# Performance work log

Measured on AMD Instinct MI355X. Metric: run time of the kernel, lower is better.

Reference implementation:

```python
import jax, jax.numpy as jnp
import numpy as np

DIM = 1024
NUM_HEADS = 16
HEAD_DIM = DIM // NUM_HEADS
SCALE = HEAD_DIM ** (-0.5)


def setup_inputs() -> dict:
    key = jax.random.key(0)
    ks = jax.random.split(key, 5)
    B, N, C = 2, 2048, DIM
    q = jax.random.normal(ks[0], (B, N, C), dtype=jnp.float32)
    k = jax.random.normal(ks[1], (B, N, C), dtype=jnp.float32)
    v = jax.random.normal(ks[2], (B, N, C), dtype=jnp.float32)
    # fused qkv Linear weight, torch layout [3*C, C]; no bias (qkv_bias=False)
    qkv_w = jax.random.normal(ks[3], (3 * C, C), dtype=jnp.float32) * (C ** -0.5)
    proj_w = jax.random.normal(ks[4], (C, C), dtype=jnp.float32) * (C ** -0.5)
    proj_b = jnp.zeros((C,), dtype=jnp.float32)
    return {"q": q, "k": k, "v": v, "qkv_w": qkv_w, "proj_w": proj_w,
            "proj_b": proj_b, "use_mask": 1}


def reference(q, k, v, qkv_w, proj_w, proj_b, use_mask):
    B, N, C = q.shape
    N_k = k.shape[1]
    H, hd = NUM_HEADS, HEAD_DIM
    # The original applies the full fused qkv Linear to each of q,k,v and keeps
    # only slice 0/1/2 respectively; computing just the used slice is identical math.
    wq, wk, wv = qkv_w[:C], qkv_w[C:2 * C], qkv_w[2 * C:]
    qh = (q @ wq.T).reshape(B, N, H, hd).transpose(0, 2, 1, 3)      # [B,H,N,hd]
    kh = (k @ wk.T).reshape(B, N_k, H, hd).transpose(0, 2, 1, 3)    # [B,H,Nk,hd]
    vh = (v @ wv.T).reshape(B, N_k, H, hd).transpose(0, 2, 1, 3)    # [B,H,Nk,hd]
    attn = jnp.einsum('bhnd,bhmd->bhnm', qh, kh) * SCALE            # [B,H,N,Nk]
    if use_mask:  # static Python flag -> causal tril mask as in the source
        msk = jnp.tril(jnp.ones((N, N_k), dtype=bool))
        attn = jnp.where(msk[None, None], attn, jnp.float32(-1e9))
    attn = jax.nn.softmax(attn, axis=-1)
    x = jnp.einsum('bhnm,bhmd->bhnd', attn, vh)                     # [B,H,N,hd]
    x = x.transpose(0, 2, 1, 3).reshape(B, N, C)
    x = x @ proj_w.T + proj_b
    return x, attn
```

## Files before the change

### kernel.cpp

```cpp
#include <hip/hip_runtime.h>


typedef unsigned short u16;
typedef unsigned int u32;
typedef __attribute__((ext_vector_type(8))) short s16x8;
typedef __attribute__((ext_vector_type(4))) float f32x4;
typedef __attribute__((ext_vector_type(4))) u16 u16x4;

#define AS1 __attribute__((address_space(1)))
#define AS3 __attribute__((address_space(3)))

static __device__ __forceinline__ u16 f2bf(float f) {
  u32 u = __builtin_bit_cast(u32, f);
  u = (u + 0x7fffu + ((u >> 16) & 1u)) >> 16;
  return (u16)u;
}

static __device__ __forceinline__ void gll16(const u16* g, u16* l) {
  __builtin_amdgcn_global_load_lds((const AS1 u32*)g, (AS3 u32*)l, 16, 0, 0);
}

static __device__ __forceinline__ f32x4 mfma_bf16(s16x8 a, s16x8 b, f32x4 c) {
  return __builtin_amdgcn_mfma_f32_16x16x32_bf16(a, b, c, 0, 0, 0);
}

__global__ __launch_bounds__(256) void cast_kernel(const float* __restrict__ in,
                                                   u16* __restrict__ out, int n4) {
  int i = blockIdx.x * 256 + threadIdx.x;
  if (i < n4) {
    f32x4 v = ((const f32x4*)in)[i];
    u16x4 o = { f2bf(v.x), f2bf(v.y), f2bf(v.z), f2bf(v.w) };
    ((u16x4*)out)[i] = o;
  }
}

static __device__ __forceinline__ void gemm_core_1024(
    const u16* __restrict__ A, const u16* __restrict__ Bm,
    int m0, int n0, int t, u16* a_s, u16* b_s, f32x4 acc[4][4]) {
  const int lane = t & 63;
  const int w = t >> 6;
  const int wm = (w & 1) * 64, wn = (w >> 1) * 64;
  const int lrow = lane & 15, lq = lane >> 4;
  const int r0 = t >> 2;
  const int c0 = (t & 3) * 8;

  for (int kt = 0; kt < 1024; kt += 32) {
    __syncthreads();
    gll16(A  + (size_t)(m0 + r0)      * 1024 + kt + c0, &a_s[(size_t)t * 8]);
    gll16(A  + (size_t)(m0 + r0 + 64) * 1024 + kt + c0, &a_s[(size_t)(t + 256) * 8]);
    gll16(Bm + (size_t)(n0 + r0)      * 1024 + kt + c0, &b_s[(size_t)t * 8]);
    gll16(Bm + (size_t)(n0 + r0 + 64) * 1024 + kt + c0, &b_s[(size_t)(t + 256) * 8]);
    __syncthreads();
    s16x8 af[4], bfr[4];
#pragma unroll
    for (int x = 0; x < 4; x++) af[x]  = *(const s16x8*)&a_s[(wm + x*16 + lrow)*32 + lq*8];
#pragma unroll
    for (int x = 0; x < 4; x++) bfr[x] = *(const s16x8*)&b_s[(wn + x*16 + lrow)*32 + lq*8];
#pragma unroll
    for (int tm = 0; tm < 4; tm++)
#pragma unroll
      for (int tn = 0; tn < 4; tn++)
        acc[tm][tn] = mfma_bf16(af[tm], bfr[tn], acc[tm][tn]);
  }
}

__global__ __launch_bounds__(256) void gemm_qkv_kernel(
    const u16* __restrict__ qb, const u16* __restrict__ kb, const u16* __restrict__ vb,
    const u16* __restrict__ wb, u16* __restrict__ Qh, u16* __restrict__ Kh,
    u16* __restrict__ Vt) {
  __shared__ u16 a_s[128*32], b_s[128*32];
  const int mode = blockIdx.z;
  const u16* A = (mode == 0) ? qb : (mode == 1) ? kb : vb;
  const u16* Bm = wb + (size_t)mode * (1024 * 1024);
  const int m0 = blockIdx.y * 128, n0 = blockIdx.x * 128;
  const int t = threadIdx.x;
  f32x4 acc[4][4];
  const f32x4 Z = {0.f, 0.f, 0.f, 0.f};
#pragma unroll
  for (int i = 0; i < 4; i++)
#pragma unroll
    for (int j = 0; j < 4; j++) acc[i][j] = Z;

  gemm_core_1024(A, Bm, m0, n0, t, a_s, b_s, acc);

  const int lane = t & 63, w = t >> 6;
  const int wm = (w & 1) * 64, wn = (w >> 1) * 64;
  const int lrow = lane & 15, lq = lane >> 4;
#pragma unroll
  for (int tm = 0; tm < 4; tm++) {
#pragma unroll
    for (int tn = 0; tn < 4; tn++) {
      const int ng = n0 + wn + tn * 16 + lrow;
      const int h = ng >> 6, d = ng & 63;
#pragma unroll
      for (int i = 0; i < 4; i++) {
        const int mg = m0 + wm + tm * 16 + lq * 4 + i;
        const int b = mg >> 11, s = mg & 2047;
        const float v = acc[tm][tn][i];
        if (mode == 0)
          Qh[((size_t)(b * 16 + h) * 2048 + s) * 64 + d] = f2bf(v * 0.125f);
        else if (mode == 1)
          Kh[((size_t)(b * 16 + h) * 2048 + s) * 64 + d] = f2bf(v);
        else
          Vt[((size_t)(b * 16 + h) * 64 + d) * 2048 + s] = f2bf(v);
      }
    }
  }
}

__global__ __launch_bounds__(256) void gemm_proj_kernel(
    const u16* __restrict__ xatt, const u16* __restrict__ pwb,
    const float* __restrict__ bias, float* __restrict__ out) {
  __shared__ u16 a_s[128*32], b_s[128*32];
  const int m0 = blockIdx.y * 128, n0 = blockIdx.x * 128;
  const int t = threadIdx.x;
  f32x4 acc[4][4];
  const f32x4 Z = {0.f, 0.f, 0.f, 0.f};
#pragma unroll
  for (int i = 0; i < 4; i++)
#pragma unroll
    for (int j = 0; j < 4; j++) acc[i][j] = Z;

  gemm_core_1024(xatt, pwb, m0, n0, t, a_s, b_s, acc);

  const int lane = t & 63, w = t >> 6;
  const int wm = (w & 1) * 64, wn = (w >> 1) * 64;
  const int lrow = lane & 15, lq = lane >> 4;
#pragma unroll
  for (int tn = 0; tn < 4; tn++) {
    const int ng = n0 + wn + tn * 16 + lrow;
    const float bv = bias[ng];
#pragma unroll
    for (int tm = 0; tm < 4; tm++) {
#pragma unroll
      for (int i = 0; i < 4; i++) {
        const int mg = m0 + wm + tm * 16 + lq * 4 + i;
        out[(size_t)mg * 1024 + ng] = acc[tm][tn][i] + bv;
      }
    }
  }
}

__global__ __launch_bounds__(256) void attn_kernel(
    const u16* __restrict__ Qh, const u16* __restrict__ Kh, const u16* __restrict__ Vt,
    float* __restrict__ attn, u16* __restrict__ xatt, const int* __restrict__ use_mask_p) {
  __shared__ u16 q_s[64*64], k_s[64*64], v_s[64*64];
  __shared__ u16 p_s[4][16*64];

  const int bh = blockIdx.y;
  const int q0 = blockIdx.x * 64;
  const int t = threadIdx.x;
  const int lane = t & 63, w = t >> 6;
  const int lrow = lane & 15, lq = lane >> 4;
  const int use_mask = *use_mask_p;
  const int T = use_mask ? (q0 >> 6) : 31;

  const int rs = t >> 3;
  const int cs = (t & 7) * 8;

  const u16* qg = Qh + ((size_t)bh * 2048 + q0) * 64;
  gll16(qg + (size_t)rs * 64 + cs,        &q_s[(size_t)t * 8]);
  gll16(qg + (size_t)(rs + 32) * 64 + cs, &q_s[(size_t)(t + 256) * 8]);
  __syncthreads();

  s16x8 qf[2];
#pragma unroll
  for (int kq = 0; kq < 2; kq++)
    qf[kq] = *(const s16x8*)&q_s[(w * 16 + lrow) * 64 + kq * 32 + lq * 8];

  const u16* kg = Kh + (size_t)bh * (2048 * 64);
  const u16* vg = Vt + (size_t)bh * (64 * 2048);

  float l_acc[4] = {0.f, 0.f, 0.f, 0.f};
  for (int tt = 0; tt <= T; tt++) {
    __syncthreads();
    gll16(kg + (size_t)(tt * 64 + rs) * 64 + cs,      &k_s[(size_t)t * 8]);
    gll16(kg + (size_t)(tt * 64 + rs + 32) * 64 + cs, &k_s[(size_t)(t + 256) * 8]);
    __syncthreads();
    f32x4 sacc[4];
    const f32x4 Z = {0.f, 0.f, 0.f, 0.f};
#pragma unroll
    for (int tn = 0; tn < 4; tn++) {
      sacc[tn] = Z;
#pragma unroll
      for (int kq = 0; kq < 2; kq++) {
        s16x8 kf = *(const s16x8*)&k_s[(tn * 16 + lrow) * 64 + kq * 32 + lq * 8];
        sacc[tn] = mfma_bf16(qf[kq], kf, sacc[tn]);
      }
    }
    const bool diag = use_mask && (tt == T);
    float part[4] = {0.f, 0.f, 0.f, 0.f};
#pragma unroll
    for (int tn = 0; tn < 4; tn++)
#pragma unroll
      for (int i = 0; i < 4; i++) {
        const bool ok = !diag || (tn * 16 + lrow <= w * 16 + lq * 4 + i);
        part[i] += ok ? __expf(sacc[tn][i]) : 0.f;
      }
#pragma unroll
    for (int i = 0; i < 4; i++) {
      float p = part[i];
      p += __shfl_xor(p, 1, 16);
      p += __shfl_xor(p, 2, 16);
      p += __shfl_xor(p, 4, 16);
      p += __shfl_xor(p, 8, 16);
      l_acc[i] += p;
    }
  }
  float inv_l[4];
#pragma unroll
  for (int i = 0; i < 4; i++) inv_l[i] = 1.0f / l_acc[i];

  f32x4 oacc[4];
  const f32x4 Z = {0.f, 0.f, 0.f, 0.f};
#pragma unroll
  for (int i = 0; i < 4; i++) oacc[i] = Z;

  for (int tt = 0; tt <= T; tt++) {
    __syncthreads();
    gll16(kg + (size_t)(tt * 64 + rs) * 64 + cs,      &k_s[(size_t)t * 8]);
    gll16(kg + (size_t)(tt * 64 + rs + 32) * 64 + cs, &k_s[(size_t)(t + 256) * 8]);
    gll16(vg + (size_t)rs * 2048 + tt * 64 + cs,        &v_s[(size_t)t * 8]);
    gll16(vg + (size_t)(rs + 32) * 2048 + tt * 64 + cs, &v_s[(size_t)(t + 256) * 8]);
    __syncthreads();
    f32x4 sacc[4];
#pragma unroll
    for (int tn = 0; tn < 4; tn++) {
      sacc[tn] = Z;
#pragma unroll
      for (int kq = 0; kq < 2; kq++) {
        s16x8 kf = *(const s16x8*)&k_s[(tn * 16 + lrow) * 64 + kq * 32 + lq * 8];
        sacc[tn] = mfma_bf16(qf[kq], kf, sacc[tn]);
      }
    }
    const bool diag = use_mask && (tt == T);
    float* abase = attn + ((size_t)(bh * 2048 + q0 + w * 16)) * 2048 + tt * 64;
#pragma unroll
    for (int tn = 0; tn < 4; tn++)
#pragma unroll
      for (int i = 0; i < 4; i++) {
        const bool ok = !diag || (tn * 16 + lrow <= w * 16 + lq * 4 + i);
        const float p = ok ? __expf(sacc[tn][i]) * inv_l[i] : 0.f;
        const int rl = lq * 4 + i;
        abase[(size_t)rl * 2048 + tn * 16 + lrow] = p;
        p_s[w][rl * 64 + tn * 16 + lrow] = f2bf(p);
      }
    s16x8 pf[2];
#pragma unroll
    for (int kq = 0; kq < 2; kq++)
      pf[kq] = *(const s16x8*)&p_s[w][lrow * 64 + kq * 32 + lq * 8];
#pragma unroll
    for (int td = 0; td < 4; td++)
#pragma unroll
      for (int kq = 0; kq < 2; kq++) {
        s16x8 vf = *(const s16x8*)&v_s[(td * 16 + lrow) * 64 + kq * 32 + lq * 8];
        oacc[td] = mfma_bf16(pf[kq], vf, oacc[td]);
      }
  }

  const int b = bh >> 4, h = bh & 15;
#pragma unroll
  for (int td = 0; td < 4; td++)
#pragma unroll
    for (int i = 0; i < 4; i++) {
      const int row = q0 + w * 16 + lq * 4 + i;
      xatt[((size_t)(b * 2048 + row)) * 1024 + h * 64 + td * 16 + lrow] = f2bf(oacc[td][i]);
    }

  if (use_mask) {
    const int zc0 = q0 + 64;
    if (zc0 < 2048) {
      const int nzv = (2048 - zc0) >> 2;
      f32x4* zb = (f32x4*)(attn + ((size_t)bh * 2048 + q0) * 2048 + zc0);
      const int row = t >> 2;
      const f32x4 Z4 = {0.f, 0.f, 0.f, 0.f};
      for (int c = (t & 3); c < nzv; c += 4)
        zb[(size_t)row * 512 + c] = Z4;
    }
  }
}

extern "C" void kernel_launch(void* const* d_in, const int* in_sizes, int n_in,
                              void* d_out, int out_size, void* d_ws, size_t ws_size,
                              hipStream_t stream) {
  const float* q      = (const float*)d_in[0];
  const float* k      = (const float*)d_in[1];
  const float* v      = (const float*)d_in[2];
  const float* qkv_w  = (const float*)d_in[3];
  const float* proj_w = (const float*)d_in[4];
  const float* proj_b = (const float*)d_in[5];
  const int*   use_mask = (const int*)d_in[6];

  const size_t MB = 1024 * 1024;
  char* ws = (char*)d_ws;
  u16* qb  = (u16*)(ws + 0 * MB);
  u16* kb  = (u16*)(ws + 8 * MB);
  u16* vb  = (u16*)(ws + 16 * MB);
  u16* wb  = (u16*)(ws + 24 * MB);
  u16* pwb = (u16*)(ws + 30 * MB);
  u16* Qh  = (u16*)(ws + 32 * MB);
  u16* Kh  = (u16*)(ws + 40 * MB);
  u16* Vt  = (u16*)(ws + 48 * MB);
  u16* xat = qb;

  float* out_x    = (float*)d_out;
  float* out_attn = out_x + (size_t)2 * 2048 * 1024;

  cast_kernel<<<4096, 256, 0, stream>>>(q, qb, 1048576);
  cast_kernel<<<4096, 256, 0, stream>>>(k, kb, 1048576);
  cast_kernel<<<4096, 256, 0, stream>>>(v, vb, 1048576);
  cast_kernel<<<3072, 256, 0, stream>>>(qkv_w, wb, 786432);
  cast_kernel<<<1024, 256, 0, stream>>>(proj_w, pwb, 262144);

  gemm_qkv_kernel<<<dim3(8, 32, 3), 256, 0, stream>>>(qb, kb, vb, wb, Qh, Kh, Vt);
  attn_kernel<<<dim3(32, 32), 256, 0, stream>>>(Qh, Kh, Vt, out_attn, xat, use_mask);
  gemm_proj_kernel<<<dim3(8, 32), 256, 0, stream>>>(xat, pwb, proj_b, out_x);
}
```

Before: 772.8 us.

## Pair causal query tiles per block with double-buffered swizzled K/V loads

Each attention block now handles two query tiles, p and 31-p, so causal work is balanced across blocks and every K/V tile loaded into LDS serves both. K and V loads are double-buffered so the next tile is fetched during compute, and LDS is XOR-swizzled, with the P scratch padded to cut bank conflicts. MFMA sections are wrapped in s_setprio. The grid is halved, which reduces block count and parallelism, and register pressure rises from holding two sets of accumulators.

```diff
diff --git a/kernel.cpp b/kernel.cpp
--- a/kernel.cpp
+++ b/kernel.cpp
@@ -141,141 +141,239 @@
   }
 }
 
+
+static __device__ __forceinline__ void qk_tile(const s16x8 qf[2], const s16x8 kf[4][2],
+                                               f32x4 sacc[4]) {
+  const f32x4 Z = {0.f, 0.f, 0.f, 0.f};
+#pragma unroll
+  for (int tn = 0; tn < 4; tn++) {
+    sacc[tn] = Z;
+#pragma unroll
+    for (int kq = 0; kq < 2; kq++)
+      sacc[tn] = mfma_bf16(qf[kq], kf[tn][kq], sacc[tn]);
+  }
+}
+
+static __device__ __forceinline__ void expsum_tile(const f32x4 sacc[4], bool diag,
+                                                   int lrow, int rbase, float l_acc[4]) {
+  float part[4] = {0.f, 0.f, 0.f, 0.f};
+#pragma unroll
+  for (int tn = 0; tn < 4; tn++)
+#pragma unroll
+    for (int i = 0; i < 4; i++) {
+      const bool ok = !diag || (tn * 16 + lrow <= rbase + i);
+      part[i] += ok ? __expf(sacc[tn][i]) : 0.f;
+    }
+#pragma unroll
+  for (int i = 0; i < 4; i++) {
+    float s = part[i];
+    s += __shfl_xor(s, 1, 16);
+    s += __shfl_xor(s, 2, 16);
+    s += __shfl_xor(s, 4, 16);
+    s += __shfl_xor(s, 8, 16);
+    l_acc[i] += s;
+  }
+}
+
+static __device__ __forceinline__ void p_tile(const f32x4 sacc[4], bool diag, int lrow,
+                                              int lq, int w, const float inv_l[4],
+                                              float* __restrict__ abase, u16* p_w,
+                                              s16x8 pf[2]) {
+#pragma unroll
+  for (int tn = 0; tn < 4; tn++)
+#pragma unroll
+    for (int i = 0; i < 4; i++) {
+      const int rl = lq * 4 + i;
+      const bool ok = !diag || (tn * 16 + lrow <= w * 16 + rl);
+      const float pv = ok ? __expf(sacc[tn][i]) * inv_l[i] : 0.f;
+      abase[(size_t)rl * 2048 + tn * 16 + lrow] = pv;
+      p_w[rl * 72 + tn * 16 + lrow] = f2bf(pv);
+    }
+#pragma unroll
+  for (int kq = 0; kq < 2; kq++)
+    pf[kq] = *(const s16x8*)&p_w[lrow * 72 + kq * 32 + lq * 8];
+}
+
 __global__ __launch_bounds__(256) void attn_kernel(
     const u16* __restrict__ Qh, const u16* __restrict__ Kh, const u16* __restrict__ Vt,
     float* __restrict__ attn, u16* __restrict__ xatt, const int* __restrict__ use_mask_p) {
-  __shared__ u16 q_s[64*64], k_s[64*64], v_s[64*64];
-  __shared__ u16 p_s[4][16*64];
+  __shared__ u16 smem[8192 + 8192 + 8 * 16 * 72];
+  u16* k_s = smem;
+  u16* vq  = smem + 8192;
+  u16* p_s = smem + 16384;
 
   const int bh = blockIdx.y;
-  const int q0 = blockIdx.x * 64;
+  const int p  = blockIdx.x;
   const int t = threadIdx.x;
   const int lane = t & 63, w = t >> 6;
   const int lrow = lane & 15, lq = lane >> 4;
   const int use_mask = *use_mask_p;
-  const int T = use_mask ? (q0 >> 6) : 31;
-
-  const int rs = t >> 3;
-  const int cs = (t & 7) * 8;
-
-  const u16* qg = Qh + ((size_t)bh * 2048 + q0) * 64;
-  gll16(qg + (size_t)rs * 64 + cs,        &q_s[(size_t)t * 8]);
-  gll16(qg + (size_t)(rs + 32) * 64 + cs, &q_s[(size_t)(t + 256) * 8]);
-  __syncthreads();
-
-  s16x8 qf[2];
-#pragma unroll
-  for (int kq = 0; kq < 2; kq++)
-    qf[kq] = *(const s16x8*)&q_s[(w * 16 + lrow) * 64 + kq * 32 + lq * 8];
+
+  const int q0[2] = { p * 64, (31 - p) * 64 };
+  const int Tc[2] = { use_mask ? p : 31, use_mask ? 31 - p : 31 };
+  const int Tmax  = Tc[1];
+
+  const int rs  = t >> 3;
+  const int csw = (((t & 7) ^ (rs & 7)) * 8);
+  const int sk  = (lrow & 7) << 3;
 
   const u16* kg = Kh + (size_t)bh * (2048 * 64);
   const u16* vg = Vt + (size_t)bh * (64 * 2048);
 
-  float l_acc[4] = {0.f, 0.f, 0.f, 0.f};
-  for (int tt = 0; tt <= T; tt++) {
+  {
+    const u16* qgA = Qh + ((size_t)bh * 2048 + q0[0]) * 64;
+    const u16* qgB = Qh + ((size_t)bh * 2048 + q0[1]) * 64;
+    gll16(qgA + (size_t)rs * 64 + csw,        &vq[t * 8]);
+    gll16(qgA + (size_t)(rs + 32) * 64 + csw, &vq[(t + 256) * 8]);
+    gll16(qgB + (size_t)rs * 64 + csw,        &vq[4096 + t * 8]);
+    gll16(qgB + (size_t)(rs + 32) * 64 + csw, &vq[4096 + (t + 256) * 8]);
+    gll16(kg + (size_t)rs * 64 + csw,         &k_s[t * 8]);
+    gll16(kg + (size_t)(rs + 32) * 64 + csw,  &k_s[(t + 256) * 8]);
+  }
+  __syncthreads();
+
+  s16x8 qf[2][2];
+  const int qrow = w * 16 + lrow;
+#pragma unroll
+  for (int kq = 0; kq < 2; kq++) {
+    qf[0][kq] = *(const s16x8*)&vq[qrow * 64 + ((kq * 32 + lq * 8) ^ sk)];
+    qf[1][kq] = *(const s16x8*)&vq[4096 + qrow * 64 + ((kq * 32 + lq * 8) ^ sk)];
+  }
+
+  const int rbase = w * 16 + lq * 4;
+
+  float l_acc[2][4];
+#pragma unroll
+  for (int c = 0; c < 2; c++)
+#pragma unroll
+    for (int i = 0; i < 4; i++) l_acc[c][i] = 0.f;
+
+  for (int tt = 0; tt <= Tmax; tt++) {
+    const int cur = tt & 1;
+    if (tt < Tmax) {
+      gll16(kg + (size_t)((tt + 1) * 64 + rs) * 64 + csw,      &k_s[(cur ^ 1) * 4096 + t * 8]);
+      gll16(kg + (size_t)((tt + 1) * 64 + rs + 32) * 64 + csw, &k_s[(cur ^ 1) * 4096 + (t + 256) * 8]);
+    }
+    s16x8 kf[4][2];
+#pragma unroll
+    for (int tn = 0; tn < 4; tn++)
+#pragma unroll
+      for (int kq = 0; kq < 2; kq++)
+        kf[tn][kq] = *(const s16x8*)&k_s[cur * 4096 + (tn * 16 + lrow) * 64 + ((kq * 32 + lq * 8) ^ sk)];
+    f32x4 sacc[4];
+    __builtin_amdgcn_s_setprio(1);
+    qk_tile(qf[1], kf, sacc);
+    __builtin_amdgcn_s_setprio(0);
+    expsum_tile(sacc, use_mask && (tt == Tc[1]), lrow, rbase, l_acc[1]);
+    if (tt <= Tc[0]) {
+      __builtin_amdgcn_s_setprio(1);
+      qk_tile(qf[0], kf, sacc);
+      __builtin_amdgcn_s_setprio(0);
+      expsum_tile(sacc, use_mask && (tt == Tc[0]), lrow, rbase, l_acc[0]);
+    }
     __syncthreads();
-    gll16(kg + (size_t)(tt * 64 + rs) * 64 + cs,      &k_s[(size_t)t * 8]);
-    gll16(kg + (size_t)(tt * 64 + rs + 32) * 64 + cs, &k_s[(size_t)(t + 256) * 8]);
+  }
+
+  float inv_l[2][4];
+#pragma unroll
+  for (int c = 0; c < 2; c++)
+#pragma unroll
+    for (int i = 0; i < 4; i++) inv_l[c][i] = 1.0f / l_acc[c][i];
+
+  f32x4 oacc[2][4];
+  const f32x4 Z = {0.f, 0.f, 0.f, 0.f};
+#pragma unroll
+  for (int c = 0; c < 2; c++)
+#pragma unroll
+    for (int i = 0; i < 4; i++) oacc[c][i] = Z;
+
+  gll16(kg + (size_t)rs * 64 + csw,          &k_s[t * 8]);
+  gll16(kg + (size_t)(rs + 32) * 64 + csw,   &k_s[(t + 256) * 8]);
+  gll16(vg + (size_t)rs * 2048 + csw,        &vq[t * 8]);
+  gll16(vg + (size_t)(rs + 32) * 2048 + csw, &vq[(t + 256) * 8]);
+  __syncthreads();
+
+  for (int tt = 0; tt <= Tmax; tt++) {
+    const int cur = tt & 1;
+    if (tt < Tmax) {
+      gll16(kg + (size_t)((tt + 1) * 64 + rs) * 64 + csw,        &k_s[(cur ^ 1) * 4096 + t * 8]);
+      gll16(kg + (size_t)((tt + 1) * 64 + rs + 32) * 64 + csw,   &k_s[(cur ^ 1) * 4096 + (t + 256) * 8]);
+      gll16(vg + (size_t)rs * 2048 + (tt + 1) * 64 + csw,        &vq[(cur ^ 1) * 4096 + t * 8]);
+      gll16(vg + (size_t)(rs + 32) * 2048 + (tt + 1) * 64 + csw, &vq[(cur ^ 1) * 4096 + (t + 256) * 8]);
+    }
+    const bool act0 = (tt <= Tc[0]);
+    s16x8 kf[4][2];
+#pragma unroll
+    for (int tn = 0; tn < 4; tn++)
+#pragma unroll
+      for (int kq = 0; kq < 2; kq++)
+        kf[tn][kq] = *(const s16x8*)&k_s[cur * 4096 + (tn * 16 + lrow) * 64 + ((kq * 32 + lq * 8) ^ sk)];
+
+    f32x4 sacc1[4], sacc0[4];
+    __builtin_amdgcn_s_setprio(1);
+    qk_tile(qf[1], kf, sacc1);
+    if (act0) qk_tile(qf[0], kf, sacc0);
+    __builtin_amdgcn_s_setprio(0);
+
+    s16x8 pf1[2], pf0[2];
+    {
+      float* abase = attn + ((size_t)(bh * 2048 + q0[1] + w * 16)) * 2048 + tt * 64;
+      p_tile(sacc1, use_mask && (tt == Tc[1]), lrow, lq, w, inv_l[1], abase,
+             p_s + (w * 2 + 1) * 1152, pf1);
+    }
+    if (act0) {
+      float* abase = attn + ((size_t)(bh * 2048 + q0[0] + w * 16)) * 2048 + tt * 64;
+      p_tile(sacc0, use_mask && (tt == Tc[0]), lrow, lq, w, inv_l[0], abase,
+             p_s + (w * 2 + 0) * 1152, pf0);
+    }
+
+    s16x8 vf[4][2];
+#pragma unroll
+    for (int td = 0; td < 4; td++)
+#pragma unroll
+      for (int kq = 0; kq < 2; kq++)
+        vf[td][kq] = *(const s16x8*)&vq[cur * 4096 + (td * 16 + lrow) * 64 + ((kq * 32 + lq * 8) ^ sk)];
+
+    __builtin_amdgcn_s_setprio(1);
+#pragma unroll
+    for (int td = 0; td < 4; td++)
+#pragma unroll
+      for (int kq = 0; kq < 2; kq++)
+        oacc[1][td] = mfma_bf16(pf1[kq], vf[td][kq], oacc[1][td]);
+    if (act0) {
+#pragma unroll
+      for (int td = 0; td < 4; td++)
+#pragma unroll
+        for (int kq = 0; kq < 2; kq++)
+          oacc[0][td] = mfma_bf16(pf0[kq], vf[td][kq], oacc[0][td]);
+    }
+    __builtin_amdgcn_s_setprio(0);
     __syncthreads();
-    f32x4 sacc[4];
-    const f32x4 Z = {0.f, 0.f, 0.f, 0.f};
-#pragma unroll
-    for (int tn = 0; tn < 4; tn++) {
-      sacc[tn] = Z;
-#pragma unroll
-      for (int kq = 0; kq < 2; kq++) {
-        s16x8 kf = *(const s16x8*)&k_s[(tn * 16 + lrow) * 64 + kq * 32 + lq * 8];
-        sacc[tn] = mfma_bf16(qf[kq], kf, sacc[tn]);
+  }
+
+  const int b = bh >> 4, h = bh & 15;
+#pragma unroll
+  for (int c = 0; c < 2; c++)
+#pragma unroll
+    for (int td = 0; td < 4; td++)
+#pragma unroll
+      for (int i = 0; i < 4; i++) {
+        const int row = q0[c] + w * 16 + lq * 4 + i;
+        xatt[((size_t)(b * 2048 + row)) * 1024 + h * 64 + td * 16 + lrow] = f2bf(oacc[c][td][i]);
       }
-    }
-    const bool diag = use_mask && (tt == T);
-    float part[4] = {0.f, 0.f, 0.f, 0.f};
-#pragma unroll
-    for (int tn = 0; tn < 4; tn++)
-#pragma unroll
-      for (int i = 0; i < 4; i++) {
-        const bool ok = !diag || (tn * 16 + lrow <= w * 16 + lq * 4 + i);
-        part[i] += ok ? __expf(sacc[tn][i]) : 0.f;
+
+  if (use_mask) {
+    const f32x4 Z4 = {0.f, 0.f, 0.f, 0.f};
+#pragma unroll
+    for (int c = 0; c < 2; c++) {
+      const int zc0 = q0[c] + 64;
+      if (zc0 < 2048) {
+        const int nzv = (2048 - zc0) >> 2;
+        f32x4* zb = (f32x4*)(attn + ((size_t)bh * 2048 + q0[c]) * 2048 + zc0);
+        const int row = t >> 2;
+        for (int cc = (t & 3); cc < nzv; cc += 4)
+          zb[(size_t)row * 512 + cc] = Z4;
       }
-#pragma unroll
-    for (int i = 0; i < 4; i++) {
-      float p = part[i];
-      p += __shfl_xor(p, 1, 16);
-      p += __shfl_xor(p, 2, 16);
-      p += __shfl_xor(p, 4, 16);
-      p += __shfl_xor(p, 8, 16);
-      l_acc[i] += p;
-    }
-  }
-  float inv_l[4];
-#pragma unroll
-  for (int i = 0; i < 4; i++) inv_l[i] = 1.0f / l_acc[i];
-
-  f32x4 oacc[4];
-  const f32x4 Z = {0.f, 0.f, 0.f, 0.f};
-#pragma unroll
-  for (int i = 0; i < 4; i++) oacc[i] = Z;
-
-  for (int tt = 0; tt <= T; tt++) {
-    __syncthreads();
-    gll16(kg + (size_t)(tt * 64 + rs) * 64 + cs,      &k_s[(size_t)t * 8]);
-    gll16(kg + (size_t)(tt * 64 + rs + 32) * 64 + cs, &k_s[(size_t)(t + 256) * 8]);
-    gll16(vg + (size_t)rs * 2048 + tt * 64 + cs,        &v_s[(size_t)t * 8]);
-    gll16(vg + (size_t)(rs + 32) * 2048 + tt * 64 + cs, &v_s[(size_t)(t + 256) * 8]);
-    __syncthreads();
-    f32x4 sacc[4];
-#pragma unroll
-    for (int tn = 0; tn < 4; tn++) {
-      sacc[tn] = Z;
-#pragma unroll
-      for (int kq = 0; kq < 2; kq++) {
-        s16x8 kf = *(const s16x8*)&k_s[(tn * 16 + lrow) * 64 + kq * 32 + lq * 8];
-        sacc[tn] = mfma_bf16(qf[kq], kf, sacc[tn]);
-      }
-    }
-    const bool diag = use_mask && (tt == T);
-    float* abase = attn + ((size_t)(bh * 2048 + q0 + w * 16)) * 2048 + tt * 64;
-#pragma unroll
-    for (int tn = 0; tn < 4; tn++)
-#pragma unroll
-      for (int i = 0; i < 4; i++) {
-        const bool ok = !diag || (tn * 16 + lrow <= w * 16 + lq * 4 + i);
-        const float p = ok ? __expf(sacc[tn][i]) * inv_l[i] : 0.f;
-        const int rl = lq * 4 + i;
-        abase[(size_t)rl * 2048 + tn * 16 + lrow] = p;
-        p_s[w][rl * 64 + tn * 16 + lrow] = f2bf(p);
-      }
-    s16x8 pf[2];
-#pragma unroll
-    for (int kq = 0; kq < 2; kq++)
-      pf[kq] = *(const s16x8*)&p_s[w][lrow * 64 + kq * 32 + lq * 8];
-#pragma unroll
-    for (int td = 0; td < 4; td++)
-#pragma unroll
-      for (int kq = 0; kq < 2; kq++) {
-        s16x8 vf = *(const s16x8*)&v_s[(td * 16 + lrow) * 64 + kq * 32 + lq * 8];
-        oacc[td] = mfma_bf16(pf[kq], vf, oacc[td]);
-      }
-  }
-
-  const int b = bh >> 4, h = bh & 15;
-#pragma unroll
-  for (int td = 0; td < 4; td++)
-#pragma unroll
-    for (int i = 0; i < 4; i++) {
-      const int row = q0 + w * 16 + lq * 4 + i;
-      xatt[((size_t)(b * 2048 + row)) * 1024 + h * 64 + td * 16 + lrow] = f2bf(oacc[td][i]);
-    }
-
-  if (use_mask) {
-    const int zc0 = q0 + 64;
-    if (zc0 < 2048) {
-      const int nzv = (2048 - zc0) >> 2;
-      f32x4* zb = (f32x4*)(attn + ((size_t)bh * 2048 + q0) * 2048 + zc0);
-      const int row = t >> 2;
-      const f32x4 Z4 = {0.f, 0.f, 0.f, 0.f};
-      for (int c = (t & 3); c < nzv; c += 4)
-        zb[(size_t)row * 512 + c] = Z4;
     }
   }
 }
@@ -313,6 +411,6 @@
   cast_kernel<<<1024, 256, 0, stream>>>(proj_w, pwb, 262144);
 
   gemm_qkv_kernel<<<dim3(8, 32, 3), 256, 0, stream>>>(qb, kb, vb, wb, Qh, Kh, Vt);
-  attn_kernel<<<dim3(32, 32), 256, 0, stream>>>(Qh, Kh, Vt, out_attn, xat, use_mask);
+  attn_kernel<<<dim3(16, 32), 256, 0, stream>>>(Qh, Kh, Vt, out_attn, xat, use_mask);
   gemm_proj_kernel<<<dim3(8, 32), 256, 0, stream>>>(xat, pwb, proj_b, out_x);
 }
```

New measurement: 729.9 us. -5.5%, faster.
